# Optimization experiments

Measured on AMD Instinct MI355X. Metric: run time of the kernel, lower is better.

## Reference

```python
import jax, jax.numpy as jnp
import numpy as np

DIM = 384
HEADS = 8


def setup_inputs() -> dict:
    key = jax.random.key(0)
    ks = jax.random.split(key, 8)
    d = DIM
    return {
        "x": jax.random.normal(ks[0], (4, d, 128, 128), jnp.float32),
        "message": jax.random.normal(ks[1], (4, d, 128, 128), jnp.float32),
        "temperature": jnp.ones((HEADS, 1, 1), jnp.float32),
        "qkv_w": jax.random.normal(ks[2], (3 * d, d), jnp.float32) * 0.02,   # 1x1 conv weight
        "dw_w": jax.random.normal(ks[3], (3 * d, 1, 3, 3), jnp.float32) * 0.02,  # depthwise 3x3
        "proj_w": jax.random.normal(ks[4], (d, d), jnp.float32) * 0.02,     # project_out 1x1
        "lin_w": jax.random.normal(ks[5], (d, 2 * d), jnp.float32) * 0.02,  # nn.Linear weight [out,in]
        "lin_b": jnp.zeros((d,), jnp.float32),
    }


def _qkv_branch(t, qkv_w, dw_w):
    # 1x1 conv (pointwise) then depthwise 3x3, groups = 3*dim
    y = jnp.einsum('oc,bchw->bohw', qkv_w, t)
    y = jax.lax.conv_general_dilated(
        y, dw_w, window_strides=(1, 1), padding='SAME',
        dimension_numbers=('NCHW', 'OIHW', 'NCHW'),
        feature_group_count=dw_w.shape[0])
    return jnp.split(y, 3, axis=1)  # q, k, v each [b, dim, h, w]


def _to_heads(t):
    b, c, h, w = t.shape
    return t.reshape(b, HEADS, c // HEADS, h * w)  # [b, head, c, n]


def _l2norm(t):
    # torch F.normalize(dim=-1, eps=1e-12)
    n = jnp.sqrt(jnp.sum(t * t, axis=-1, keepdims=True))
    return t / jnp.maximum(n, 1e-12)


def reference(x, message, temperature, qkv_w, dw_w, proj_w, lin_w, lin_b):
    b, c, h, w = x.shape
    q, k, v = (_to_heads(t) for t in _qkv_branch(x, qkv_w, dw_w))
    q_m, k_m, v_m = (_to_heads(t) for t in _qkv_branch(message, qkv_w, dw_w))

    k_c = jnp.concatenate([k, k_m], axis=2)   # [b, head, 2c, n]
    v_c = jnp.concatenate([v, v_m], axis=2)

    q = _l2norm(q)
    k_c = _l2norm(k_c)
    q_m = _l2norm(q_m)

    # channel attention: [b, head, c, 2c]
    attn1 = jax.nn.softmax(jnp.einsum('bhcn,bhdn->bhcd', q, k_c) * temperature, axis=-1)
    attn2 = jax.nn.softmax(jnp.einsum('bhcn,bhdn->bhcd', q_m, k_c) * temperature, axis=-1)

    out1 = jnp.einsum('bhcd,bhdn->bhcn', attn1, v_c)  # [b, head, c, n]
    out2 = jnp.einsum('bhcd,bhdn->bhcn', attn2, v_c)

    # 'b head c (h w) -> b (h w) (head c)'
    out1 = out1.transpose(0, 3, 1, 2).reshape(b, h * w, c)
    out2 = out2.transpose(0, 3, 1, 2).reshape(b, h * w, c)

    cat = jnp.concatenate([out1, out2], axis=2)  # [b, n, 2c]
    out = cat @ lin_w.T + lin_b                  # [b, n, c]

    # 'b (h w) c -> b c h w'
    out = out.transpose(0, 2, 1).reshape(b, c, h, w)
    out = jnp.einsum('oc,bchw->bohw', proj_w, out)
    return out
```

## Files before the change

### kernel.cpp

```cpp
#include <hip/hip_runtime.h>

typedef unsigned short u16;
typedef unsigned int u32;

#define BATCH 4
#define CDIM 384
#define IMG 128
#define HW 16384
#define QKVC 1152
#define NHEADS 8
#define CHD 48
#define DD2 96
#define KFIN 768

typedef __attribute__((ext_vector_type(8))) short bf16x8;
typedef __attribute__((ext_vector_type(4))) float f32x4;

__device__ __forceinline__ u16 f2bf(float f){
  union { float f; u32 u; } v; v.f = f;
  u32 u = v.u;
  u32 r = (u + 0x7fffu + ((u >> 16) & 1u)) >> 16;
  return (u16)r;
}
__device__ __forceinline__ float bf2f(u16 h){
  union { u32 u; float f; } v; v.u = ((u32)h) << 16;
  return v.f;
}

#define OFF_QKVX  ((size_t)0)
#define OFF_QKVM  ((size_t)150994944)
#define OFF_T     ((size_t)301989888)
#define OFF_SSQ   ((size_t)339738624)
#define OFF_S     ((size_t)339775488)
#define OFF_ATTN  ((size_t)340955136)
#define OFF_AFINB ((size_t)342134784)
#define OFF_W2    ((size_t)344494080)
#define OFF_B2    ((size_t)345673728)
#define OFF_WB    ((size_t)345675264)

typedef __attribute__((address_space(1))) const u32 gas_u32;
typedef __attribute__((address_space(3))) u32 las_u32;
__device__ __forceinline__ void gl_lds16(const u16* g, u16* l){
  __builtin_amdgcn_global_load_lds((gas_u32*)g, (las_u32*)l, 16, 0, 0);
}

__device__ __forceinline__ u16* t_row(u16* T0, u16* qkvm, int par, int ch){
  if (par == 0) return T0 + (size_t)ch * HW;
  int bq = ch / 384;
  int rr = ch - bq * 384;
  return qkvm + ((size_t)bq * QKVC + 2 * CDIM + rr) * HW;
}

__global__ void __launch_bounds__(256) k_w2(const float* __restrict__ proj,
                                            const float* __restrict__ lin,
                                            const float* __restrict__ linb,
                                            const float* __restrict__ qkvw,
                                            float* __restrict__ W2,
                                            float* __restrict__ b2,
                                            u16* __restrict__ Wb){
  int idx = blockIdx.x * 256 + threadIdx.x;
  if (idx < CDIM * KFIN){
    int o = idx / KFIN, d = idx % KFIN;
    float acc = 0.f;
    for (int c = 0; c < CDIM; c++)
      acc = fmaf(proj[o * CDIM + c], lin[c * KFIN + d], acc);
    W2[idx] = acc;
  }
  if (idx < CDIM){
    float acc = 0.f;
    for (int c = 0; c < CDIM; c++)
      acc = fmaf(proj[idx * CDIM + c], linb[c], acc);
    b2[idx] = acc;
  }
  if (idx < QKVC * CDIM) Wb[idx] = f2bf(qkvw[idx]);
}

__device__ __forceinline__ void loadrow(const u16* __restrict__ src, int r, int cg, float* o){
  if ((unsigned)r >= IMG){
    #pragma unroll
    for (int i = 0; i < 18; i++) o[i] = 0.f;
    return;
  }
  const u16* p = src + (size_t)r * IMG + cg * 16;
  uint4 v0 = *(const uint4*)p;
  uint4 v1 = *(const uint4*)(p + 8);
  u32 ww[8] = {v0.x, v0.y, v0.z, v0.w, v1.x, v1.y, v1.z, v1.w};
  #pragma unroll
  for (int i = 0; i < 8; i++){
    union { u32 u; float f; } lo, hi;
    lo.u = ww[i] << 16;
    hi.u = ww[i] & 0xffff0000u;
    o[1 + 2 * i] = lo.f;
    o[2 + 2 * i] = hi.f;
  }
  o[0]  = (cg > 0) ? bf2f(p[-1]) : 0.f;
  o[17] = (cg < 7) ? bf2f(p[16]) : 0.f;
}

__global__ void __launch_bounds__(256) k_stage(
    int t, int npw, int ndw,
    const u16* __restrict__ Wb, u16* __restrict__ Bt,
    u16* __restrict__ T0, u16* __restrict__ qkvx, u16* __restrict__ qkvm,
    const float* __restrict__ x, const float* __restrict__ msg,
    const float* __restrict__ dww, float* __restrict__ ssq){
  __shared__ __align__(16) u16 smem[16384];
  int bid = blockIdx.x;
  int tid = threadIdx.x;

  if (bid < npw){
    int z = t - 1, par = z & 1;
    const u16* B = Bt + (size_t)z * HW * CDIM;
    u16* As = smem;
    u16* Bs = smem + 8192;
    int swz = (bid & 7) * 144 + (bid >> 3);
    int bx = swz % 9, by = swz / 9;
    int m0 = bx * 128, n0 = by * 128;
    int w = tid >> 6, lane = tid & 63;
    int wy = w >> 1, wx = w & 1;
    int lm = lane & 15, q = lane >> 4;

    int srow = w * 16 + (lane >> 2);
    int scol = (lane & 3) * 8;
    const u16* ga = Wb + (size_t)(m0 + srow) * CDIM + scol;
    const u16* gb = B + (size_t)(n0 + srow) * CDIM + scol;
    u16* la = As + srow * 32 + scol;
    u16* lb = Bs + srow * 32 + scol;

    f32x4 acc[4][4];
    #pragma unroll
    for (int i = 0; i < 4; i++)
      #pragma unroll
      for (int j = 0; j < 4; j++) acc[i][j] = (f32x4){0.f,0.f,0.f,0.f};

#define PW_STAGE(buf, k0) do{ \
      gl_lds16(ga + (k0),             la + (buf) * 4096); \
      gl_lds16(ga + 64*CDIM + (k0),   la + (buf) * 4096 + 2048); \
      gl_lds16(gb + (k0),             lb + (buf) * 4096); \
      gl_lds16(gb + 64*CDIM + (k0),   lb + (buf) * 4096 + 2048); \
    }while(0)

    PW_STAGE(0, 0);
    __syncthreads();
    int cur = 0;
    for (int kt = 0; kt < 12; kt++){
      if (kt < 11) PW_STAGE(cur ^ 1, (kt + 1) * 32);
      bf16x8 af[4], bfr[4];
      #pragma unroll
      for (int i = 0; i < 4; i++)
        af[i] = *(const bf16x8*)&As[cur * 4096 + (wy * 64 + i * 16 + lm) * 32 + q * 8];
      #pragma unroll
      for (int j = 0; j < 4; j++)
        bfr[j] = *(const bf16x8*)&Bs[cur * 4096 + (wx * 64 + j * 16 + lm) * 32 + q * 8];
      #pragma unroll
      for (int i = 0; i < 4; i++)
        #pragma unroll
        for (int j = 0; j < 4; j++)
          acc[i][j] = __builtin_amdgcn_mfma_f32_16x16x32_bf16(af[i], bfr[j], acc[i][j], 0, 0, 0);
      __syncthreads();
      cur ^= 1;
    }
#undef PW_STAGE
    #pragma unroll
    for (int i = 0; i < 4; i++){
      #pragma unroll
      for (int r = 0; r < 4; r++){
        int row = m0 + wy * 64 + i * 16 + q * 4 + r;
        u16* cp = t_row(T0, qkvm, par, row) + n0 + wx * 64 + lm;
        #pragma unroll
        for (int j = 0; j < 4; j++)
          cp[j * 16] = f2bf(acc[i][j][r]);
      }
    }

  } else if (bid < npw + ndw){
    int ch = bid - npw;
    int z = t - 2, par = z & 1;
    const u16* src = t_row(T0, qkvm, par, ch);
    u16* dst;
    if (ch < 2 * CDIM){
      u16* qd = ((z >> 2) ? qkvm : qkvx) + (size_t)(z & 3) * QKVC * HW;
      dst = qd + (size_t)ch * HW;
    } else {
      dst = Bt + (size_t)z * HW * CDIM + (size_t)(ch - 2 * CDIM) * HW;
    }
    float w[9];
    #pragma unroll
    for (int t9 = 0; t9 < 9; t9++) w[t9] = dww[ch * 9 + t9];
    int rg = tid >> 3, cg = tid & 7;
    int r0 = rg * 4;
    float ra[18], rb[18], rc[18];
    loadrow(src, r0 - 1, cg, ra);
    loadrow(src, r0,     cg, rb);
    float ss = 0.f;
    #pragma unroll
    for (int rr = 0; rr < 4; rr++){
      int r = r0 + rr;
      loadrow(src, r + 1, cg, rc);
      u32 pk[8];
      #pragma unroll
      for (int xx = 0; xx < 16; xx++){
        float a2 = w[0] * ra[xx];
        a2 = fmaf(w[1], ra[xx + 1], a2);
        a2 = fmaf(w[2], ra[xx + 2], a2);
        a2 = fmaf(w[3], rb[xx],     a2);
        a2 = fmaf(w[4], rb[xx + 1], a2);
        a2 = fmaf(w[5], rb[xx + 2], a2);
        a2 = fmaf(w[6], rc[xx],     a2);
        a2 = fmaf(w[7], rc[xx + 1], a2);
        a2 = fmaf(w[8], rc[xx + 2], a2);
        ss = fmaf(a2, a2, ss);
        u16 hv = f2bf(a2);
        if (xx & 1) pk[xx >> 1] |= (u32)hv << 16;
        else        pk[xx >> 1]  = (u32)hv;
      }
      *(uint4*)(dst + (size_t)r * IMG + cg * 16)     = *(uint4*)&pk[0];
      *(uint4*)(dst + (size_t)r * IMG + cg * 16 + 8) = *(uint4*)&pk[4];
      #pragma unroll
      for (int ii = 0; ii < 18; ii++){ ra[ii] = rb[ii]; rb[ii] = rc[ii]; }
    }
    if (ch < 2 * CDIM){
      float* red = (float*)smem;
      red[tid] = ss;
      __syncthreads();
      for (int s = 128; s > 0; s >>= 1){
        if (tid < s) red[tid] += red[tid + s];
        __syncthreads();
      }
      if (tid == 0) ssq[(size_t)z * QKVC + ch] = red[0];
    }

  } else {
    int cb = bid - npw - ndw;
    int z = t;
    const float* src = (z < 4 ? x : msg) + (size_t)(z & 3) * CDIM * HW;
    u16* dstz = Bt + (size_t)z * HW * CDIM;
    int n0 = (cb & 127) * 128;
    int c0 = (cb >> 7) * 64;
    u16 (*tile)[130] = (u16(*)[130])smem;
    #pragma unroll
    for (int i = 0; i < 8; i++){
      int c = (tid >> 5) + i * 8;
      int nq = tid & 31;
      float4 v = *(const float4*)(src + (size_t)(c0 + c) * HW + n0 + nq * 4);
      u32 p0 = (u32)f2bf(v.x) | ((u32)f2bf(v.y) << 16);
      u32 p1 = (u32)f2bf(v.z) | ((u32)f2bf(v.w) << 16);
      *(u32*)&tile[c][nq * 4]     = p0;
      *(u32*)&tile[c][nq * 4 + 2] = p1;
    }
    __syncthreads();
    #pragma unroll
    for (int u = 0; u < 2; u++){
      int idx = tid + u * 256;
      int n = idx >> 2, j = idx & 3;
      u32 pk[8];
      #pragma unroll
      for (int p = 0; p < 8; p++)
        pk[p] = (u32)tile[j * 16 + 2 * p][n] | ((u32)tile[j * 16 + 2 * p + 1][n] << 16);
      u16* dp = dstz + (size_t)(n0 + n) * CDIM + c0 + j * 16;
      *(uint4*)dp       = *(uint4*)&pk[0];
      *(uint4*)(dp + 8) = *(uint4*)&pk[4];
    }
  }
}

#define LCHUNK 1024
__global__ void __launch_bounds__(256) k_tail(u16* __restrict__ qkvx,
                                              u16* __restrict__ qkvm,
                                              float* __restrict__ S,
                                              const u16* __restrict__ Bt){
  __shared__ u16 tile[48][136];
  int bid = blockIdx.x;
  int tid = threadIdx.x;

  if (bid < 512){
    int nc = bid & 15;
    int bh = bid >> 4;
    int b = bh & 3, h = bh >> 2;
    int w = tid >> 6, lane = tid & 63;
    int wy = w >> 1, wx = w & 1;
    int lm = lane & 15, quad = lane >> 4;

    const u16* ap[3]; const u16* bp[3];
    #pragma unroll
    for (int i = 0; i < 3; i++){
      int g = wy * 48 + i * 16 + lm;
      int c = (g < 48) ? g : g - 48;
      ap[i] = ((g < 48) ? qkvx : qkvm) + ((size_t)b * QKVC + h * CHD + c) * HW;
      int d = wx * 48 + i * 16 + lm;
      int cc = (d < 48) ? d : d - 48;
      bp[i] = ((d < 48) ? qkvx : qkvm) + ((size_t)b * QKVC + CDIM + h * CHD + cc) * HW;
    }
    f32x4 acc[3][3];
    #pragma unroll
    for (int i = 0; i < 3; i++)
      #pragma unroll
      for (int j = 0; j < 3; j++) acc[i][j] = (f32x4){0.f,0.f,0.f,0.f};

    int nbeg = nc * LCHUNK + quad * 8;
    int nend = nc * LCHUNK + LCHUNK;
    for (int n = nbeg; n < nend; n += 64){
      bf16x8 af0[3], bf0[3], af1[3], bf1[3];
      #pragma unroll
      for (int i = 0; i < 3; i++){
        af0[i] = *(const bf16x8*)(ap[i] + n);
        af1[i] = *(const bf16x8*)(ap[i] + n + 32);
      }
      #pragma unroll
      for (int j = 0; j < 3; j++){
        bf0[j] = *(const bf16x8*)(bp[j] + n);
        bf1[j] = *(const bf16x8*)(bp[j] + n + 32);
      }
      #pragma unroll
      for (int i = 0; i < 3; i++)
        #pragma unroll
        for (int j = 0; j < 3; j++)
          acc[i][j] = __builtin_amdgcn_mfma_f32_16x16x32_bf16(af0[i], bf0[j], acc[i][j], 0, 0, 0);
      #pragma unroll
      for (int i = 0; i < 3; i++)
        #pragma unroll
        for (int j = 0; j < 3; j++)
          acc[i][j] = __builtin_amdgcn_mfma_f32_16x16x32_bf16(af1[i], bf1[j], acc[i][j], 0, 0, 0);
    }
    #pragma unroll
    for (int i = 0; i < 3; i++){
      #pragma unroll
      for (int r = 0; r < 4; r++){
        int g = wy * 48 + i * 16 + quad * 4 + r;
        int iq = (g >= 48) ? 1 : 0;
        int c = iq ? g - 48 : g;
        float* Sp = S + (((size_t)(iq * BATCH + b) * NHEADS + h) * CHD + c) * DD2;
        #pragma unroll
        for (int j = 0; j < 3; j++)
          atomicAdd(&Sp[wx * 48 + j * 16 + lm], acc[i][j][r]);
      }
    }
  } else {
    int v = bid - 512;
    int nb = v & 127;
    int h = (v >> 7) & 7;
    int z = v >> 10;
    int inp = z >> 2, b = z & 3;
    const u16* vcn = Bt + (size_t)z * HW * CDIM;
    int n0 = nb * 128;
    u16* vt = (h < 4 ? qkvx : qkvm) + ((size_t)b * QKVC + 2 * CDIM) * HW;
    int dbase = (h & 3) * 96 + inp * 48;
    #pragma unroll
    for (int j = 0; j < 3; j++){
      int i = tid + j * 256;
      int row = i >> 4, c8 = i & 15;
      uint4 vv = *(const uint4*)(vcn + (size_t)(h * 48 + row) * HW + n0 + c8 * 8);
      *(uint4*)&tile[row][c8 * 8] = vv;
    }
    __syncthreads();
    int n = tid >> 1, half = tid & 1;
    u16* dstp = vt + (size_t)(n0 + n) * CDIM + dbase + half * 24;
    #pragma unroll
    for (int u = 0; u < 3; u++){
      u32 pk[4];
      #pragma unroll
      for (int p = 0; p < 4; p++){
        int c = half * 24 + u * 8 + p * 2;
        pk[p] = (u32)tile[c][n] | ((u32)tile[c + 1][n] << 16);
      }
      *(uint4*)(dstp + u * 8) = *(uint4*)pk;
    }
  }
}

__global__ void __launch_bounds__(128) k_softmax(const float* __restrict__ S,
                                                 const float* __restrict__ ssq,
                                                 const float* __restrict__ temp,
                                                 float* __restrict__ attn){
  int row = blockIdx.x;
  int c = row % CHD;
  int h = (row / CHD) % NHEADS;
  int b = (row / (CHD * NHEADS)) % BATCH;
  int iq = row / (CHD * NHEADS * BATCH);
  int tid = threadIdx.x;
  __shared__ float sh[128];
  const float* Sp = S + (size_t)row * DD2;
  float ssq_q = ssq[(iq * BATCH + b) * QKVC + h * CHD + c];
  float nq = fmaxf(sqrtf(ssq_q), 1e-12f);
  float tmp = temp[h];
  float logit = -1e30f;
  int d = tid;
  if (d < DD2){
    float ssq_k = ssq[((d < CHD ? 0 : 1) * BATCH + b) * QKVC + CDIM + h * CHD + (d % CHD)];
    float nk = fmaxf(sqrtf(ssq_k), 1e-12f);
    logit = Sp[d] * tmp / (nq * nk);
  }
  sh[tid] = logit; __syncthreads();
  for (int s = 64; s > 0; s >>= 1){
    if (tid < s) sh[tid] = fmaxf(sh[tid], sh[tid + s]);
    __syncthreads();
  }
  float mx = sh[0]; __syncthreads();
  float e = (d < DD2) ? expf(logit - mx) : 0.f;
  sh[tid] = e; __syncthreads();
  for (int s = 64; s > 0; s >>= 1){
    if (tid < s) sh[tid] += sh[tid + s];
    __syncthreads();
  }
  float sum = sh[0];
  if (d < DD2) attn[(size_t)row * DD2 + d] = e / sum;
}

__global__ void __launch_bounds__(128) k_mmat(const float* __restrict__ attn,
                                              const float* __restrict__ W2,
                                              u16* __restrict__ AfinB){
  int oz = blockIdx.x;
  int h = blockIdx.y;
  int b = blockIdx.z;
  __shared__ float a1[CHD * DD2];
  __shared__ float a2[CHD * DD2];
  int tid = threadIdx.x;
  const float* A1 = attn + ((size_t)(0 * BATCH + b) * NHEADS + h) * CHD * DD2;
  const float* A2 = attn + ((size_t)(1 * BATCH + b) * NHEADS + h) * CHD * DD2;
  for (int i = tid; i < CHD * DD2; i += 128){ a1[i] = A1[i]; a2[i] = A2[i]; }
  __syncthreads();
  int e = tid;
  if (e < DD2){
    for (int oo = 0; oo < 8; oo++){
      int o = oz * 8 + oo;
      float acc = 0.f;
      #pragma unroll 4
      for (int cc = 0; cc < CHD; cc++){
        acc = fmaf(W2[o * KFIN + h * CHD + cc],        a1[cc * DD2 + e], acc);
        acc = fmaf(W2[o * KFIN + CDIM + h * CHD + cc], a2[cc * DD2 + e], acc);
      }
      AfinB[((size_t)b * CDIM + o) * KFIN + h * DD2 + e] = f2bf(acc);
    }
  }
}

__global__ void __launch_bounds__(256) k_fin(const u16* __restrict__ AfB,
                                             const u16* __restrict__ qkvx,
                                             const u16* __restrict__ qkvm,
                                             const float* __restrict__ b2,
                                             float* __restrict__ out){
  __shared__ __align__(16) u16 As[2 * 4096];
  __shared__ __align__(16) u16 Bs[2 * 4096];
  int orig = blockIdx.x;
  int swz = (orig & 7) * 192 + (orig >> 3);
  int m = swz % 3;
  int rest = swz / 3;
  int n0 = (rest & 127) * 128;
  int bz = rest >> 7;
  int m0 = m * 128;
  int tid = threadIdx.x;
  int w = tid >> 6, lane = tid & 63;
  int wy = w >> 1, wx = w & 1;
  int lm = lane & 15, q = lane >> 4;

  int srow = w * 16 + (lane >> 2);
  int scol = (lane & 3) * 8;
  const u16* A = AfB + (size_t)bz * CDIM * KFIN;
  const u16* ga  = A + (size_t)(m0 + srow) * KFIN + scol;
  const u16* gb0 = qkvx + ((size_t)bz * QKVC + 2 * CDIM) * HW + (size_t)(n0 + srow) * CDIM + scol;
  const u16* gb1 = qkvm + ((size_t)bz * QKVC + 2 * CDIM) * HW + (size_t)(n0 + srow) * CDIM + scol;
  u16* la = As + srow * 32 + scol;
  u16* lb = Bs + srow * 32 + scol;

  f32x4 acc[4][4];
  #pragma unroll
  for (int i = 0; i < 4; i++)
    #pragma unroll
    for (int j = 0; j < 4; j++) acc[i][j] = (f32x4){0.f,0.f,0.f,0.f};

#define FIN_STAGE(buf, t) do{ \
    int hp_ = (t) >= 12; \
    int k0_ = ((t) - hp_ * 12) * 32; \
    const u16* gb_ = hp_ ? gb1 : gb0; \
    gl_lds16(ga + hp_ * CDIM + k0_,            la + (buf) * 4096); \
    gl_lds16(ga + hp_ * CDIM + k0_ + 64*KFIN,  la + (buf) * 4096 + 2048); \
    gl_lds16(gb_ + k0_,                        lb + (buf) * 4096); \
    gl_lds16(gb_ + k0_ + 64*CDIM,              lb + (buf) * 4096 + 2048); \
  }while(0)

  FIN_STAGE(0, 0);
  __syncthreads();
  int cur = 0;
  for (int t = 0; t < 24; t++){
    if (t < 23) FIN_STAGE(cur ^ 1, t + 1);
    bf16x8 af[4], bfr[4];
    #pragma unroll
    for (int i = 0; i < 4; i++)
      af[i] = *(const bf16x8*)&As[cur * 4096 + (wy * 64 + i * 16 + lm) * 32 + q * 8];
    #pragma unroll
    for (int j = 0; j < 4; j++)
      bfr[j] = *(const bf16x8*)&Bs[cur * 4096 + (wx * 64 + j * 16 + lm) * 32 + q * 8];
    #pragma unroll
    for (int i = 0; i < 4; i++)
      #pragma unroll
      for (int j = 0; j < 4; j++)
        acc[i][j] = __builtin_amdgcn_mfma_f32_16x16x32_bf16(af[i], bfr[j], acc[i][j], 0, 0, 0);
    __syncthreads();
    cur ^= 1;
  }
#undef FIN_STAGE
  #pragma unroll
  for (int i = 0; i < 4; i++){
    #pragma unroll
    for (int r = 0; r < 4; r++){
      int row = m0 + wy * 64 + i * 16 + q * 4 + r;
      float bv = b2[row];
      float* cp = out + (size_t)bz * CDIM * HW + (size_t)row * HW + n0 + wx * 64 + lm;
      #pragma unroll
      for (int j = 0; j < 4; j++)
        cp[j * 16] = acc[i][j][r] + bv;
    }
  }
}

extern "C" void kernel_launch(void* const* d_in, const int* in_sizes, int n_in,
                              void* d_out, int out_size, void* d_ws, size_t ws_size,
                              hipStream_t stream){
  const float* x      = (const float*)d_in[0];
  const float* msg    = (const float*)d_in[1];
  const float* temp   = (const float*)d_in[2];
  const float* qkv_w  = (const float*)d_in[3];
  const float* dw_w   = (const float*)d_in[4];
  const float* proj_w = (const float*)d_in[5];
  const float* lin_w  = (const float*)d_in[6];
  const float* lin_b  = (const float*)d_in[7];
  float* out = (float*)d_out;

  char* ws = (char*)d_ws;
  u16*   qkvx  = (u16*)(ws + OFF_QKVX);
  u16*   qkvm  = (u16*)(ws + OFF_QKVM);
  u16*   T0    = (u16*)(ws + OFF_T);
  float* ssq   = (float*)(ws + OFF_SSQ);
  float* S     = (float*)(ws + OFF_S);
  float* attn  = (float*)(ws + OFF_ATTN);
  u16*   AfinB = (u16*)(ws + OFF_AFINB);
  float* W2    = (float*)(ws + OFF_W2);
  float* b2    = (float*)(ws + OFF_B2);
  u16*   Wb    = (u16*)(ws + OFF_WB);

  u16* Bt = (u16*)d_out;

  hipMemsetAsync(ws + OFF_S, 0, (OFF_ATTN - OFF_S), stream);

  k_w2<<<dim3((QKVC * CDIM + 255) / 256), dim3(256), 0, stream>>>(
      proj_w, lin_w, lin_b, qkv_w, W2, b2, Wb);

  for (int t = 0; t < 10; t++){
    int npw  = (t >= 1 && t <= 8) ? 1152 : 0;
    int ndw  = (t >= 2) ? 1152 : 0;
    int ncvt = (t < 8) ? 768 : 0;
    k_stage<<<dim3(npw + ndw + ncvt), dim3(256), 0, stream>>>(
        t, npw, ndw, Wb, Bt, T0, qkvx, qkvm, x, msg, dw_w, ssq);
  }

  k_tail<<<dim3(512 + 8192), dim3(256), 0, stream>>>(qkvx, qkvm, S, Bt);
  k_softmax<<<dim3(2 * BATCH * NHEADS * CHD), dim3(128), 0, stream>>>(S, ssq, temp, attn);
  k_mmat<<<dim3(CDIM / 8, NHEADS, BATCH), dim3(128), 0, stream>>>(attn, W2, AfinB);
  k_fin<<<dim3(3 * (HW / 128) * BATCH), dim3(256), 0, stream>>>(
      AfinB, qkvx, qkvm, b2, out);
}
```

Baseline: 816.8 us.

## Interleave V-transpose work into staged pipeline and split tail reduction finer

Moves most of the V transpose blocks from the tail kernel into the staged pipeline launches, scheduling each (z, head) slice as soon as its depthwise output is available, and flips the T0 buffer parity accordingly. Only the last slice's transpose remains in the tail kernel. The QK^T reduction in the tail is split into 32 chunks of 512 instead of 16 of 1024 to raise parallelism, at the cost of more atomic adds. The aim is to fill idle CUs during stages and shorten the serial tail, but the schedule depends on subtle buffer-reuse ordering that could race if misjudged.

```diff
diff --git a/kernel.cpp b/kernel.cpp
--- a/kernel.cpp
+++ b/kernel.cpp
@@ -45,7 +45,7 @@
 }
 
 __device__ __forceinline__ u16* t_row(u16* T0, u16* qkvm, int par, int ch){
-  if (par == 0) return T0 + (size_t)ch * HW;
+  if (par == 1) return T0 + (size_t)ch * HW;
   int bq = ch / 384;
   int rr = ch - bq * 384;
   return qkvm + ((size_t)bq * QKVC + 2 * CDIM + rr) * HW;
@@ -98,7 +98,7 @@
 }
 
 __global__ void __launch_bounds__(256) k_stage(
-    int t, int npw, int ndw,
+    int t, int npw, int ndw, int ncvt,
     const u16* __restrict__ Wb, u16* __restrict__ Bt,
     u16* __restrict__ T0, u16* __restrict__ qkvx, u16* __restrict__ qkvm,
     const float* __restrict__ x, const float* __restrict__ msg,
@@ -229,7 +229,7 @@
       if (tid == 0) ssq[(size_t)z * QKVC + ch] = red[0];
     }
 
-  } else {
+  } else if (bid < npw + ndw + ncvt){
     int cb = bid - npw - ndw;
     int z = t;
     const float* src = (z < 4 ? x : msg) + (size_t)(z & 3) * CDIM * HW;
@@ -260,10 +260,52 @@
       *(uint4*)dp       = *(uint4*)&pk[0];
       *(uint4*)(dp + 8) = *(uint4*)&pk[4];
     }
-  }
-}
-
-#define LCHUNK 1024
+
+  } else {
+    int iv = bid - npw - ndw - ncvt;
+    int z, h;
+    if (t < 9){
+      if (iv < 512){ z = t - 3; h = iv >> 7; }
+      else         { z = 3;     h = 4 + ((iv - 512) >> 7); }
+    } else {
+      if (iv < 512){ z = 6; h = iv >> 7; }
+      else {
+        int u = iv - 512;
+        int zi = u >> 9;
+        z = (zi < 3) ? zi : zi + 1;
+        h = 4 + ((u >> 7) & 3);
+      }
+    }
+    int nb = iv & 127;
+    int inp = z >> 2, b = z & 3;
+    const u16* vcn = Bt + (size_t)z * HW * CDIM;
+    int n0 = nb * 128;
+    u16* vt = (h < 4 ? qkvx : qkvm) + ((size_t)b * QKVC + 2 * CDIM) * HW;
+    int dbase = (h & 3) * 96 + inp * 48;
+    u16 (*tile)[136] = (u16(*)[136])smem;
+    #pragma unroll
+    for (int j = 0; j < 3; j++){
+      int i = tid + j * 256;
+      int row = i >> 4, c8 = i & 15;
+      uint4 vv = *(const uint4*)(vcn + (size_t)(h * 48 + row) * HW + n0 + c8 * 8);
+      *(uint4*)&tile[row][c8 * 8] = vv;
+    }
+    __syncthreads();
+    int n = tid >> 1, half = tid & 1;
+    u16* dstp = vt + (size_t)(n0 + n) * CDIM + dbase + half * 24;
+    #pragma unroll
+    for (int u = 0; u < 3; u++){
+      u32 pk[4];
+      #pragma unroll
+      for (int p = 0; p < 4; p++){
+        int c = half * 24 + u * 8 + p * 2;
+        pk[p] = (u32)tile[c][n] | ((u32)tile[c + 1][n] << 16);
+      }
+      *(uint4*)(dstp + u * 8) = *(uint4*)pk;
+    }
+  }
+}
+
 __global__ void __launch_bounds__(256) k_tail(u16* __restrict__ qkvx,
                                               u16* __restrict__ qkvm,
                                               float* __restrict__ S,
@@ -272,9 +314,9 @@
   int bid = blockIdx.x;
   int tid = threadIdx.x;
 
-  if (bid < 512){
-    int nc = bid & 15;
-    int bh = bid >> 4;
+  if (bid < 1024){
+    int nc = bid & 31;
+    int bh = bid >> 5;
     int b = bh & 3, h = bh >> 2;
     int w = tid >> 6, lane = tid & 63;
     int wy = w >> 1, wx = w & 1;
@@ -296,8 +338,8 @@
       #pragma unroll
       for (int j = 0; j < 3; j++) acc[i][j] = (f32x4){0.f,0.f,0.f,0.f};
 
-    int nbeg = nc * LCHUNK + quad * 8;
-    int nend = nc * LCHUNK + LCHUNK;
+    int nbeg = nc * 512 + quad * 8;
+    int nend = nc * 512 + 512;
     for (int n = nbeg; n < nend; n += 64){
       bf16x8 af0[3], bf0[3], af1[3], bf1[3];
       #pragma unroll
@@ -335,10 +377,10 @@
       }
     }
   } else {
-    int v = bid - 512;
+    int v = bid - 1024;
     int nb = v & 127;
-    int h = (v >> 7) & 7;
-    int z = v >> 10;
+    int h = v >> 7;
+    int z = 7;
     int inp = z >> 2, b = z & 3;
     const u16* vcn = Bt + (size_t)z * HW * CDIM;
     int n0 = nb * 128;
@@ -548,11 +590,14 @@
     int npw  = (t >= 1 && t <= 8) ? 1152 : 0;
     int ndw  = (t >= 2) ? 1152 : 0;
     int ncvt = (t < 8) ? 768 : 0;
-    k_stage<<<dim3(npw + ndw + ncvt), dim3(256), 0, stream>>>(
-        t, npw, ndw, Wb, Bt, T0, qkvx, qkvm, x, msg, dw_w, ssq);
-  }
-
-  k_tail<<<dim3(512 + 8192), dim3(256), 0, stream>>>(qkvx, qkvm, S, Bt);
+    int nvt  = 0;
+    if (t >= 3 && t <= 8) nvt = (t == 6) ? 1024 : 512;
+    if (t == 9) nvt = 3584;
+    k_stage<<<dim3(npw + ndw + ncvt + nvt), dim3(256), 0, stream>>>(
+        t, npw, ndw, ncvt, Wb, Bt, T0, qkvx, qkvm, x, msg, dw_w, ssq);
+  }
+
+  k_tail<<<dim3(1024 + 1024), dim3(256), 0, stream>>>(qkvx, qkvm, S, Bt);
   k_softmax<<<dim3(2 * BATCH * NHEADS * CHD), dim3(128), 0, stream>>>(S, ssq, temp, attn);
   k_mmat<<<dim3(CDIM / 8, NHEADS, BATCH), dim3(128), 0, stream>>>(attn, W2, AfinB);
   k_fin<<<dim3(3 * (HW / 128) * BATCH), dim3(256), 0, stream>>>(
```

Result: slower. 848.7 us (+3.9%).

## Overlap Gram-matrix logits for early batches with final depthwise stage

Applied to the files above, without the earlier changes.

Moves the q·k logits computation for batches 0-2 into the last pipeline stage launch (t=9), running alongside the final depthwise conv blocks, and leaves only batch 3 in the tail kernel. The chunk size is halved to 512 to give more blocks. This aims to fill idle GPU capacity in the final stage and shrink the tail kernel's critical path, in exchange for more atomic adds into S and a dependency on those batches' q/k already being finished by t=9.

```diff
diff --git a/kernel.cpp b/kernel.cpp
--- a/kernel.cpp
+++ b/kernel.cpp
@@ -98,21 +98,87 @@
 }
 
 __global__ void __launch_bounds__(256) k_stage(
-    int t, int npw, int ndw,
+    int t, int nlog, int npw, int ndw,
     const u16* __restrict__ Wb, u16* __restrict__ Bt,
     u16* __restrict__ T0, u16* __restrict__ qkvx, u16* __restrict__ qkvm,
     const float* __restrict__ x, const float* __restrict__ msg,
-    const float* __restrict__ dww, float* __restrict__ ssq){
+    const float* __restrict__ dww, float* __restrict__ ssq,
+    float* __restrict__ S){
   __shared__ __align__(16) u16 smem[16384];
   int bid = blockIdx.x;
   int tid = threadIdx.x;
 
-  if (bid < npw){
+  if (bid < nlog){
+    int idx = bid;
+    int b = idx >> 8;
+    int nc = idx & 31;
+    int h = (idx >> 5) & 7;
+    int w = tid >> 6, lane = tid & 63;
+    int wy = w >> 1, wx = w & 1;
+    int lm = lane & 15, quad = lane >> 4;
+
+    const u16* ap[3]; const u16* bp[3];
+    #pragma unroll
+    for (int i = 0; i < 3; i++){
+      int g = wy * 48 + i * 16 + lm;
+      int c = (g < 48) ? g : g - 48;
+      ap[i] = ((g < 48) ? qkvx : qkvm) + ((size_t)b * QKVC + h * CHD + c) * HW;
+      int d = wx * 48 + i * 16 + lm;
+      int cc = (d < 48) ? d : d - 48;
+      bp[i] = ((d < 48) ? qkvx : qkvm) + ((size_t)b * QKVC + CDIM + h * CHD + cc) * HW;
+    }
+    f32x4 acc[3][3];
+    #pragma unroll
+    for (int i = 0; i < 3; i++)
+      #pragma unroll
+      for (int j = 0; j < 3; j++) acc[i][j] = (f32x4){0.f,0.f,0.f,0.f};
+
+    int nbeg = nc * 512 + quad * 8;
+    int nend = nc * 512 + 512;
+    for (int n = nbeg; n < nend; n += 64){
+      bf16x8 af0[3], bf0[3], af1[3], bf1[3];
+      #pragma unroll
+      for (int i = 0; i < 3; i++){
+        af0[i] = *(const bf16x8*)(ap[i] + n);
+        af1[i] = *(const bf16x8*)(ap[i] + n + 32);
+      }
+      #pragma unroll
+      for (int j = 0; j < 3; j++){
+        bf0[j] = *(const bf16x8*)(bp[j] + n);
+        bf1[j] = *(const bf16x8*)(bp[j] + n + 32);
+      }
+      #pragma unroll
+      for (int i = 0; i < 3; i++)
+        #pragma unroll
+        for (int j = 0; j < 3; j++)
+          acc[i][j] = __builtin_amdgcn_mfma_f32_16x16x32_bf16(af0[i], bf0[j], acc[i][j], 0, 0, 0);
+      #pragma unroll
+      for (int i = 0; i < 3; i++)
+        #pragma unroll
+        for (int j = 0; j < 3; j++)
+          acc[i][j] = __builtin_amdgcn_mfma_f32_16x16x32_bf16(af1[i], bf1[j], acc[i][j], 0, 0, 0);
+    }
+    #pragma unroll
+    for (int i = 0; i < 3; i++){
+      #pragma unroll
+      for (int r = 0; r < 4; r++){
+        int g = wy * 48 + i * 16 + quad * 4 + r;
+        int iq = (g >= 48) ? 1 : 0;
+        int c = iq ? g - 48 : g;
+        float* Sp = S + (((size_t)(iq * BATCH + b) * NHEADS + h) * CHD + c) * DD2;
+        #pragma unroll
+        for (int j = 0; j < 3; j++)
+          atomicAdd(&Sp[wx * 48 + j * 16 + lm], acc[i][j][r]);
+      }
+    }
+
+  } else if (bid < nlog + npw){
+    int pb = bid - nlog;
     int z = t - 1, par = z & 1;
     const u16* B = Bt + (size_t)z * HW * CDIM;
     u16* As = smem;
     u16* Bs = smem + 8192;
-    int swz = (bid & 7) * 144 + (bid >> 3);
+    int swz = (pb & 7) * 144 + (pb >> 3);
     int bx = swz % 9, by = swz / 9;
     int m0 = bx * 128, n0 = by * 128;
     int w = tid >> 6, lane = tid & 63;
@@ -172,8 +238,8 @@
       }
     }
 
-  } else if (bid < npw + ndw){
-    int ch = bid - npw;
+  } else if (bid < nlog + npw + ndw){
+    int ch = bid - nlog - npw;
     int z = t - 2, par = z & 1;
     const u16* src = t_row(T0, qkvm, par, ch);
     u16* dst;
@@ -230,7 +296,7 @@
     }
 
   } else {
-    int cb = bid - npw - ndw;
+    int cb = bid - nlog - npw - ndw;
     int z = t;
     const float* src = (z < 4 ? x : msg) + (size_t)(z & 3) * CDIM * HW;
     u16* dstz = Bt + (size_t)z * HW * CDIM;
@@ -263,7 +329,6 @@
   }
 }
 
-#define LCHUNK 1024
 __global__ void __launch_bounds__(256) k_tail(u16* __restrict__ qkvx,
                                               u16* __restrict__ qkvm,
                                               float* __restrict__ S,
@@ -272,10 +337,10 @@
   int bid = blockIdx.x;
   int tid = threadIdx.x;
 
-  if (bid < 512){
-    int nc = bid & 15;
-    int bh = bid >> 4;
-    int b = bh & 3, h = bh >> 2;
+  if (bid < 256){
+    int b = 3;
+    int nc = bid & 31;
+    int h = bid >> 5;
     int w = tid >> 6, lane = tid & 63;
     int wy = w >> 1, wx = w & 1;
     int lm = lane & 15, quad = lane >> 4;
@@ -296,8 +361,8 @@
       #pragma unroll
       for (int j = 0; j < 3; j++) acc[i][j] = (f32x4){0.f,0.f,0.f,0.f};
 
-    int nbeg = nc * LCHUNK + quad * 8;
-    int nend = nc * LCHUNK + LCHUNK;
+    int nbeg = nc * 512 + quad * 8;
+    int nend = nc * 512 + 512;
     for (int n = nbeg; n < nend; n += 64){
       bf16x8 af0[3], bf0[3], af1[3], bf1[3];
       #pragma unroll
@@ -335,7 +400,7 @@
       }
     }
   } else {
-    int v = bid - 512;
+    int v = bid - 256;
     int nb = v & 127;
     int h = (v >> 7) & 7;
     int z = v >> 10;
@@ -545,14 +610,15 @@
       proj_w, lin_w, lin_b, qkv_w, W2, b2, Wb);
 
   for (int t = 0; t < 10; t++){
+    int nlog = (t == 9) ? 768 : 0;
     int npw  = (t >= 1 && t <= 8) ? 1152 : 0;
     int ndw  = (t >= 2) ? 1152 : 0;
     int ncvt = (t < 8) ? 768 : 0;
-    k_stage<<<dim3(npw + ndw + ncvt), dim3(256), 0, stream>>>(
-        t, npw, ndw, Wb, Bt, T0, qkvx, qkvm, x, msg, dw_w, ssq);
-  }
-
-  k_tail<<<dim3(512 + 8192), dim3(256), 0, stream>>>(qkvx, qkvm, S, Bt);
+    k_stage<<<dim3(nlog + npw + ndw + ncvt), dim3(256), 0, stream>>>(
+        t, nlog, npw, ndw, Wb, Bt, T0, qkvx, qkvm, x, msg, dw_w, ssq, S);
+  }
+
+  k_tail<<<dim3(256 + 8192), dim3(256), 0, stream>>>(qkvx, qkvm, S, Bt);
   k_softmax<<<dim3(2 * BATCH * NHEADS * CHD), dim3(128), 0, stream>>>(S, ssq, temp, attn);
   k_mmat<<<dim3(CDIM / 8, NHEADS, BATCH), dim3(128), 0, stream>>>(attn, W2, AfinB);
   k_fin<<<dim3(3 * (HW / 128) * BATCH), dim3(256), 0, stream>>>(
```

Result: no change. 821.2 us (+0.5%).
